# Kernel tuning notes

Hardware: AMD Instinct MI355X
Metric: run time of the kernel (lower is better)

## Reference

```python
import jax, jax.numpy as jnp
import numpy as np

TEMPERATURE = 0.1  # use_temperature=True


def setup_inputs() -> dict:
    key = jax.random.key(0)
    # encoder output features: [batch_size, num_epoch, feature_dim]
    feature = jax.random.normal(key, (128, 64, 128), dtype=jnp.float32)
    return {"feature": feature}


def reference(feature):
    # L2-normalize along feature dim (F.normalize, p=2, dim=1 on flat features)
    f = feature / jnp.linalg.norm(feature, axis=-1, keepdims=True)
    B, E, D = f.shape
    # full pairwise logits: [B, E, E, B]
    logits = jnp.einsum('ijk,mnk->ijnm', f, f) / TEMPERATURE
    e = jnp.exp(logits)
    idx = jnp.arange(B)
    # mask[i, j, :, i] = 1 -> positives are the m == i block: e[i, j, :, i]
    pos = e[idx, :, :, idx].sum(-1)              # [B, E]
    neg = e.sum(axis=(2, 3)) - pos               # [B, E] everything else
    loss = (-jnp.log(pos / (pos + neg))).mean()
    return loss
```

## Files before the change

kernel.cpp:

```cpp
#include <hip/hip_runtime.h>
#include <hip/hip_bf16.h>

#define N_ROWS 8192
#define DIM    128
#define TILE   128
#define CPG    8
#define EXPTEN 22026.465794806718f
#define SCALE  3.7982826f

typedef __attribute__((ext_vector_type(8))) short short8;
typedef __attribute__((ext_vector_type(4))) float floatx4;

#if __has_builtin(__builtin_amdgcn_exp2f)
#define EXP2F(x) __builtin_amdgcn_exp2f(x)
#else
#define EXP2F(x) __expf((x) * 0.6931471805599453f)
#endif

__global__ void norm_kernel(const float* __restrict__ F, __hip_bfloat16* __restrict__ Xb,
                            float* __restrict__ pos, float* __restrict__ den) {
    int lane = threadIdx.x & 63;
    int wave = threadIdx.x >> 6;
    int row  = blockIdx.x * 4 + wave;
    const float2 v = *(const float2*)(F + (size_t)row * DIM + lane * 2);
    float ss = v.x * v.x + v.y * v.y;
    #pragma unroll
    for (int m = 1; m < 64; m <<= 1) ss += __shfl_xor(ss, m);
    float inv = rsqrtf(ss) * SCALE;
    __hip_bfloat162 o;
    o.x = __float2bfloat16(v.x * inv);
    o.y = __float2bfloat16(v.y * inv);
    *((__hip_bfloat162*)(Xb + (size_t)row * DIM) + lane) = o;
    if (lane == 0) { pos[row] = 0.f; den[row] = 0.f; }
}

__global__ __launch_bounds__(256, 2) void gram_kernel(
        const __hip_bfloat16* __restrict__ Xb,
        float* __restrict__ pos, float* __restrict__ den) {
    const int tid  = threadIdx.x;
    const int rb   = blockIdx.x;
    const int cg   = blockIdx.y;
    const int lane = tid & 63;
    const int wave = tid >> 6;
    const int wm   = wave >> 1, wn = wave & 1;
    const int quad = lane >> 4;
    const int l15  = lane & 15;

    short8 af[4][4];
    {
        const __hip_bfloat16* Ab = Xb + ((size_t)(rb * TILE + wm * 64 + l15)) * DIM + quad * 8;
        #pragma unroll
        for (int mi = 0; mi < 4; ++mi)
            #pragma unroll
            for (int ko = 0; ko < 4; ++ko)
                af[mi][ko] = *(const short8*)(Ab + mi * 16 * DIM + ko * 32);
    }

    float dp[4][4];
    #pragma unroll
    for (int a = 0; a < 4; ++a)
        #pragma unroll
        for (int b = 0; b < 4; ++b) dp[a][b] = 0.f;

    floatx4 acc[4][4];
    short8 bfr[4][4];

    auto epilogue = [&](int ct) {
        const bool pos_tile = (ct == rb) && (wm == wn);
        #pragma unroll
        for (int mi = 0; mi < 4; ++mi)
            #pragma unroll
            for (int rg = 0; rg < 4; ++rg) {
                float dadd = 0.f;
                #pragma unroll
                for (int ni = 0; ni < 4; ++ni)
                    dadd += EXP2F(acc[mi][ni][rg]);
                if (pos_tile) {
                    if (l15 == quad * 4 + rg)
                        dadd += EXPTEN - EXP2F(acc[mi][mi][rg]);
                    float p = dadd;
                    #pragma unroll
                    for (int m = 1; m < 16; m <<= 1) p += __shfl_xor(p, m);
                    if (l15 == 0)
                        atomicAdd(&pos[rb * TILE + wm * 64 + mi * 16 + quad * 4 + rg], p);
                }
                dp[mi][rg] += dadd;
            }
    };

    auto load_b = [&](int ct) {
        const __hip_bfloat16* Bb = Xb + ((size_t)(ct * TILE + wn * 64 + l15)) * DIM + quad * 8;
        #pragma unroll
        for (int ni = 0; ni < 4; ++ni)
            #pragma unroll
            for (int ko = 0; ko < 4; ++ko)
                bfr[ni][ko] = *(const short8*)(Bb + ni * 16 * DIM + ko * 32);
    };

    auto do_mfma = [&]() {
        #pragma unroll
        for (int mi = 0; mi < 4; ++mi)
            #pragma unroll
            for (int ni = 0; ni < 4; ++ni) acc[mi][ni] = (floatx4)0.0f;
        #pragma unroll
        for (int ko = 0; ko < 4; ++ko)
            #pragma unroll
            for (int mi = 0; mi < 4; ++mi)
                #pragma unroll
                for (int ni = 0; ni < 4; ++ni)
                    acc[mi][ni] = __builtin_amdgcn_mfma_f32_16x16x32_bf16(
                        af[mi][ko], bfr[ni][ko], acc[mi][ni], 0, 0, 0);
    };

    load_b(cg * CPG);
    do_mfma();
    #pragma unroll 1
    for (int t = 1; t < CPG; ++t) {
        load_b(cg * CPG + t);
        epilogue(cg * CPG + t - 1);
        do_mfma();
    }
    epilogue(cg * CPG + CPG - 1);

    #pragma unroll
    for (int mi = 0; mi < 4; ++mi)
        #pragma unroll
        for (int rg = 0; rg < 4; ++rg) {
            float d = dp[mi][rg];
            #pragma unroll
            for (int m = 1; m < 16; m <<= 1) d += __shfl_xor(d, m);
            if (l15 == 0)
                atomicAdd(&den[rb * TILE + wm * 64 + mi * 16 + quad * 4 + rg], d);
        }
}

__global__ void loss_kernel(const float* __restrict__ pos, const float* __restrict__ den,
                            float* __restrict__ out) {
    __shared__ float red[4];
    float acc = 0.f;
    for (int i = threadIdx.x; i < N_ROWS / 4; i += 256) {
        float4 d = ((const float4*)den)[i];
        float4 p = ((const float4*)pos)[i];
        acc += __logf(d.x / p.x) + __logf(d.y / p.y) +
               __logf(d.z / p.z) + __logf(d.w / p.w);
    }
    #pragma unroll
    for (int m = 1; m < 64; m <<= 1) acc += __shfl_xor(acc, m);
    int lane = threadIdx.x & 63, w = threadIdx.x >> 6;
    if (lane == 0) red[w] = acc;
    __syncthreads();
    if (threadIdx.x == 0)
        out[0] = (red[0] + red[1] + red[2] + red[3]) * (1.0f / (float)N_ROWS);
}

extern "C" void kernel_launch(void* const* d_in, const int* in_sizes, int n_in,
                              void* d_out, int out_size, void* d_ws, size_t ws_size,
                              hipStream_t stream) {
    const float* feature = (const float*)d_in[0];
    float* pos = (float*)d_ws;
    float* den = pos + N_ROWS;
    __hip_bfloat16* Xb = (__hip_bfloat16*)(den + N_ROWS);

    norm_kernel<<<N_ROWS / 4, 256, 0, stream>>>(feature, Xb, pos, den);
    gram_kernel<<<dim3(64, 8), 256, 0, stream>>>(Xb, pos, den);
    loss_kernel<<<1, 256, 0, stream>>>(pos, den, (float*)d_out);
}
```

Measured before the change: 99.97 us.

## Stage B tiles through swizzled LDS double buffer with direct global-to-LDS loads

Replaces the per-wave register loads of the B tile with a double-buffered shared-memory stage filled by global_load_lds DMA, using an XOR swizzle to avoid bank conflicts. Each wave now reads its B fragments from LDS, so the two waves sharing a column half no longer each fetch the same data from global memory, and the next tile's load overlaps the current tile's MFMA and exp epilogue. This costs 64KB of LDS per block, which may limit occupancy to two blocks per CU, and adds a barrier per tile. The unconditional use of the exp2 builtin also drops the fallback path.

```diff
diff --git a/kernel.cpp b/kernel.cpp
--- a/kernel.cpp
+++ b/kernel.cpp
@@ -11,11 +11,12 @@
 typedef __attribute__((ext_vector_type(8))) short short8;
 typedef __attribute__((ext_vector_type(4))) float floatx4;
 
-#if __has_builtin(__builtin_amdgcn_exp2f)
 #define EXP2F(x) __builtin_amdgcn_exp2f(x)
-#else
-#define EXP2F(x) __expf((x) * 0.6931471805599453f)
-#endif
+
+#define GLOAD_LDS(g, l)                                                        \
+    __builtin_amdgcn_global_load_lds(                                          \
+        (const __attribute__((address_space(1))) void*)(g),                    \
+        (__attribute__((address_space(3))) void*)(l), 16, 0, 0)
 
 __global__ void norm_kernel(const float* __restrict__ F, __hip_bfloat16* __restrict__ Xb,
                             float* __restrict__ pos, float* __restrict__ den) {
@@ -37,6 +38,7 @@
 __global__ __launch_bounds__(256, 2) void gram_kernel(
         const __hip_bfloat16* __restrict__ Xb,
         float* __restrict__ pos, float* __restrict__ den) {
+    __shared__ __hip_bfloat16 Bs[2][TILE * DIM];
     const int tid  = threadIdx.x;
     const int rb   = blockIdx.x;
     const int cg   = blockIdx.y;
@@ -62,10 +64,43 @@
         #pragma unroll
         for (int b = 0; b < 4; ++b) dp[a][b] = 0.f;
 
-    floatx4 acc[4][4];
-    short8 bfr[4][4];
+    auto stage = [&](int ct, int buf) {
+        #pragma unroll
+        for (int i = 0; i < 8; ++i) {
+            int chunk = (i * 4 + wave) * 64 + lane;
+            int r  = chunk >> 4;
+            int cs = (chunk & 15) ^ (r & 15);
+            const __hip_bfloat16* gp = Xb + ((size_t)(ct * TILE + r)) * DIM + cs * 8;
+            char* lp = (char*)&Bs[buf][0] + (i * 4 + wave) * 1024;
+            GLOAD_LDS(gp, lp);
+        }
+    };
 
-    auto epilogue = [&](int ct) {
+    auto compute = [&](int ct, int buf) {
+        floatx4 acc[4][4];
+        #pragma unroll
+        for (int mi = 0; mi < 4; ++mi)
+            #pragma unroll
+            for (int ni = 0; ni < 4; ++ni) acc[mi][ni] = (floatx4)0.0f;
+
+        const char* Bb = (const char*)&Bs[buf][0];
+        #pragma unroll
+        for (int ko = 0; ko < 4; ++ko) {
+            short8 bf[4];
+            #pragma unroll
+            for (int ni = 0; ni < 4; ++ni) {
+                int r  = wn * 64 + ni * 16 + l15;
+                int ch = (ko * 4 + quad) ^ l15;
+                bf[ni] = *(const short8*)(Bb + r * 256 + ch * 16);
+            }
+            #pragma unroll
+            for (int mi = 0; mi < 4; ++mi)
+                #pragma unroll
+                for (int ni = 0; ni < 4; ++ni)
+                    acc[mi][ni] = __builtin_amdgcn_mfma_f32_16x16x32_bf16(
+                        af[mi][ko], bf[ni], acc[mi][ni], 0, 0, 0);
+        }
+
         const bool pos_tile = (ct == rb) && (wm == wn);
         #pragma unroll
         for (int mi = 0; mi < 4; ++mi)
@@ -88,39 +123,15 @@
             }
     };
 
-    auto load_b = [&](int ct) {
-        const __hip_bfloat16* Bb = Xb + ((size_t)(ct * TILE + wn * 64 + l15)) * DIM + quad * 8;
-        #pragma unroll
-        for (int ni = 0; ni < 4; ++ni)
-            #pragma unroll
-            for (int ko = 0; ko < 4; ++ko)
-                bfr[ni][ko] = *(const short8*)(Bb + ni * 16 * DIM + ko * 32);
-    };
-
-    auto do_mfma = [&]() {
-        #pragma unroll
-        for (int mi = 0; mi < 4; ++mi)
-            #pragma unroll
-            for (int ni = 0; ni < 4; ++ni) acc[mi][ni] = (floatx4)0.0f;
-        #pragma unroll
-        for (int ko = 0; ko < 4; ++ko)
-            #pragma unroll
-            for (int mi = 0; mi < 4; ++mi)
-                #pragma unroll
-                for (int ni = 0; ni < 4; ++ni)
-                    acc[mi][ni] = __builtin_amdgcn_mfma_f32_16x16x32_bf16(
-                        af[mi][ko], bfr[ni][ko], acc[mi][ni], 0, 0, 0);
-    };
-
-    load_b(cg * CPG);
-    do_mfma();
+    stage(cg * CPG, 0);
+    __syncthreads();
     #pragma unroll 1
-    for (int t = 1; t < CPG; ++t) {
-        load_b(cg * CPG + t);
-        epilogue(cg * CPG + t - 1);
-        do_mfma();
+    for (int t = 0; t < CPG - 1; ++t) {
+        stage(cg * CPG + t + 1, (t + 1) & 1);
+        compute(cg * CPG + t, t & 1);
+        __syncthreads();
     }
-    epilogue(cg * CPG + CPG - 1);
+    compute(cg * CPG + CPG - 1, (CPG - 1) & 1);
 
     #pragma unroll
     for (int mi = 0; mi < 4; ++mi)
```

After: 87.69 us. 1.14x faster.

## Restructure gram kernel: per-wave 64-row strips, 24 column groups, atomic-free partial reduction

Applied to the files above, without the earlier changes.

Each wave now owns a separate 64-row strip and streams 16-column B fragments with a one-step register prefetch. The grid changes from 64x8 to 32x24 with an uneven 5/6-tile column split, to fill the GPU better, and occupancy rises to 3 blocks per SIMD. The atomicAdd reductions into den and pos are replaced by plain per-group partial writes, summed afterwards by a new dr_kernel and a tiny final loss kernel. This removes the atomics and the zero-init, at the cost of an extra launch and more workspace traffic.

```diff
diff --git a/kernel.cpp b/kernel.cpp
--- a/kernel.cpp
+++ b/kernel.cpp
@@ -3,22 +3,16 @@
 
 #define N_ROWS 8192
 #define DIM    128
-#define TILE   128
-#define CPG    8
+#define NGRP   24
 #define EXPTEN 22026.465794806718f
 #define SCALE  3.7982826f
 
 typedef __attribute__((ext_vector_type(8))) short short8;
 typedef __attribute__((ext_vector_type(4))) float floatx4;
 
-#if __has_builtin(__builtin_amdgcn_exp2f)
 #define EXP2F(x) __builtin_amdgcn_exp2f(x)
-#else
-#define EXP2F(x) __expf((x) * 0.6931471805599453f)
-#endif
 
-__global__ void norm_kernel(const float* __restrict__ F, __hip_bfloat16* __restrict__ Xb,
-                            float* __restrict__ pos, float* __restrict__ den) {
+__global__ void norm_kernel(const float* __restrict__ F, __hip_bfloat16* __restrict__ Xb) {
     int lane = threadIdx.x & 63;
     int wave = threadIdx.x >> 6;
     int row  = blockIdx.x * 4 + wave;
@@ -31,24 +25,28 @@
     o.x = __float2bfloat16(v.x * inv);
     o.y = __float2bfloat16(v.y * inv);
     *((__hip_bfloat162*)(Xb + (size_t)row * DIM) + lane) = o;
-    if (lane == 0) { pos[row] = 0.f; den[row] = 0.f; }
 }
 
-__global__ __launch_bounds__(256, 2) void gram_kernel(
+__global__ __launch_bounds__(256, 3) void gram_kernel(
         const __hip_bfloat16* __restrict__ Xb,
-        float* __restrict__ pos, float* __restrict__ den) {
-    const int tid  = threadIdx.x;
+        float* __restrict__ pos, float* __restrict__ part) {
     const int rb   = blockIdx.x;
     const int cg   = blockIdx.y;
-    const int lane = tid & 63;
-    const int wave = tid >> 6;
-    const int wm   = wave >> 1, wn = wave & 1;
+    const int lane = threadIdx.x & 63;
+    const int wave = threadIdx.x >> 6;
     const int quad = lane >> 4;
     const int l15  = lane & 15;
 
+    const int start  = (cg < 16) ? cg * 5 : 80 + (cg - 16) * 6;
+    const int cnt    = (cg < 16) ? 5 : 6;
+    const int nsteps = cnt * 4;
+    const int c0     = start * 64;
+
+    const int R0 = rb * 256 + wave * 64;
+
     short8 af[4][4];
     {
-        const __hip_bfloat16* Ab = Xb + ((size_t)(rb * TILE + wm * 64 + l15)) * DIM + quad * 8;
+        const __hip_bfloat16* Ab = Xb + (size_t)(R0 + l15) * DIM + quad * 8;
         #pragma unroll
         for (int mi = 0; mi < 4; ++mi)
             #pragma unroll
@@ -56,112 +54,118 @@
                 af[mi][ko] = *(const short8*)(Ab + mi * 16 * DIM + ko * 32);
     }
 
-    float dp[4][4];
+    const __hip_bfloat16* Bb = Xb + (size_t)(c0 + l15) * DIM + quad * 8;
+
+    float dp[4][4], pp[4][4];
     #pragma unroll
     for (int a = 0; a < 4; ++a)
         #pragma unroll
-        for (int b = 0; b < 4; ++b) dp[a][b] = 0.f;
+        for (int b = 0; b < 4; ++b) { dp[a][b] = 0.f; pp[a][b] = 0.f; }
 
-    floatx4 acc[4][4];
-    short8 bfr[4][4];
+    const int  pt     = R0 >> 6;
+    const bool haspos = (pt >= start) && (pt < start + cnt);
+    const int  s0     = (pt - start) * 4;
 
-    auto epilogue = [&](int ct) {
-        const bool pos_tile = (ct == rb) && (wm == wn);
+    short8 nb[4];
+    #pragma unroll
+    for (int ko = 0; ko < 4; ++ko)
+        nb[ko] = *(const short8*)(Bb + ko * 32);
+
+    #pragma unroll 1
+    for (int s = 0; s < nsteps; ++s) {
+        short8 cb[4];
+        #pragma unroll
+        for (int ko = 0; ko < 4; ++ko) cb[ko] = nb[ko];
+        if (s + 1 < nsteps) {
+            const __hip_bfloat16* p = Bb + (size_t)(s + 1) * 16 * DIM;
+            #pragma unroll
+            for (int ko = 0; ko < 4; ++ko)
+                nb[ko] = *(const short8*)(p + ko * 32);
+        }
+
+        floatx4 acc[4];
+        #pragma unroll
+        for (int mi = 0; mi < 4; ++mi) acc[mi] = (floatx4)0.0f;
+        #pragma unroll
+        for (int ko = 0; ko < 4; ++ko)
+            #pragma unroll
+            for (int mi = 0; mi < 4; ++mi)
+                acc[mi] = __builtin_amdgcn_mfma_f32_16x16x32_bf16(
+                    af[mi][ko], cb[ko], acc[mi], 0, 0, 0);
+
+        const bool ispos = haspos && (s >= s0) && (s < s0 + 4);
         #pragma unroll
         for (int mi = 0; mi < 4; ++mi)
             #pragma unroll
             for (int rg = 0; rg < 4; ++rg) {
-                float dadd = 0.f;
-                #pragma unroll
-                for (int ni = 0; ni < 4; ++ni)
-                    dadd += EXP2F(acc[mi][ni][rg]);
-                if (pos_tile) {
-                    if (l15 == quad * 4 + rg)
-                        dadd += EXPTEN - EXP2F(acc[mi][mi][rg]);
-                    float p = dadd;
-                    #pragma unroll
-                    for (int m = 1; m < 16; m <<= 1) p += __shfl_xor(p, m);
-                    if (l15 == 0)
-                        atomicAdd(&pos[rb * TILE + wm * 64 + mi * 16 + quad * 4 + rg], p);
-                }
-                dp[mi][rg] += dadd;
+                float ev = EXP2F(acc[mi][rg]);
+                if (ispos && mi == s - s0 && l15 == quad * 4 + rg)
+                    ev = EXPTEN;
+                dp[mi][rg] += ev;
+                if (ispos) pp[mi][rg] += ev;
             }
-    };
-
-    auto load_b = [&](int ct) {
-        const __hip_bfloat16* Bb = Xb + ((size_t)(ct * TILE + wn * 64 + l15)) * DIM + quad * 8;
-        #pragma unroll
-        for (int ni = 0; ni < 4; ++ni)
-            #pragma unroll
-            for (int ko = 0; ko < 4; ++ko)
-                bfr[ni][ko] = *(const short8*)(Bb + ni * 16 * DIM + ko * 32);
-    };
-
-    auto do_mfma = [&]() {
-        #pragma unroll
-        for (int mi = 0; mi < 4; ++mi)
-            #pragma unroll
-            for (int ni = 0; ni < 4; ++ni) acc[mi][ni] = (floatx4)0.0f;
-        #pragma unroll
-        for (int ko = 0; ko < 4; ++ko)
-            #pragma unroll
-            for (int mi = 0; mi < 4; ++mi)
-                #pragma unroll
-                for (int ni = 0; ni < 4; ++ni)
-                    acc[mi][ni] = __builtin_amdgcn_mfma_f32_16x16x32_bf16(
-                        af[mi][ko], bfr[ni][ko], acc[mi][ni], 0, 0, 0);
-    };
-
-    load_b(cg * CPG);
-    do_mfma();
-    #pragma unroll 1
-    for (int t = 1; t < CPG; ++t) {
-        load_b(cg * CPG + t);
-        epilogue(cg * CPG + t - 1);
-        do_mfma();
     }
-    epilogue(cg * CPG + CPG - 1);
 
     #pragma unroll
     for (int mi = 0; mi < 4; ++mi)
         #pragma unroll
         for (int rg = 0; rg < 4; ++rg) {
-            float d = dp[mi][rg];
+            float v = dp[mi][rg];
             #pragma unroll
-            for (int m = 1; m < 16; m <<= 1) d += __shfl_xor(d, m);
+            for (int m = 1; m < 16; m <<= 1) v += __shfl_xor(v, m);
             if (l15 == 0)
-                atomicAdd(&den[rb * TILE + wm * 64 + mi * 16 + quad * 4 + rg], d);
+                part[(size_t)cg * N_ROWS + R0 + mi * 16 + quad * 4 + rg] = v;
         }
+    if (haspos) {
+        #pragma unroll
+        for (int mi = 0; mi < 4; ++mi)
+            #pragma unroll
+            for (int rg = 0; rg < 4; ++rg) {
+                float v = pp[mi][rg];
+                #pragma unroll
+                for (int m = 1; m < 16; m <<= 1) v += __shfl_xor(v, m);
+                if (l15 == 0)
+                    pos[R0 + mi * 16 + quad * 4 + rg] = v;
+            }
+    }
 }
 
-__global__ void loss_kernel(const float* __restrict__ pos, const float* __restrict__ den,
-                            float* __restrict__ out) {
+__global__ void dr_kernel(const float* __restrict__ part, const float* __restrict__ pos,
+                          float* __restrict__ bsum) {
     __shared__ float red[4];
-    float acc = 0.f;
-    for (int i = threadIdx.x; i < N_ROWS / 4; i += 256) {
-        float4 d = ((const float4*)den)[i];
-        float4 p = ((const float4*)pos)[i];
-        acc += __logf(d.x / p.x) + __logf(d.y / p.y) +
-               __logf(d.z / p.z) + __logf(d.w / p.w);
-    }
+    const int row = blockIdx.x * 256 + threadIdx.x;
+    float den = 0.f;
     #pragma unroll
-    for (int m = 1; m < 64; m <<= 1) acc += __shfl_xor(acc, m);
+    for (int g = 0; g < NGRP; ++g)
+        den += part[(size_t)g * N_ROWS + row];
+    float v = __logf(den / pos[row]);
+    #pragma unroll
+    for (int m = 1; m < 64; m <<= 1) v += __shfl_xor(v, m);
     int lane = threadIdx.x & 63, w = threadIdx.x >> 6;
-    if (lane == 0) red[w] = acc;
+    if (lane == 0) red[w] = v;
     __syncthreads();
     if (threadIdx.x == 0)
-        out[0] = (red[0] + red[1] + red[2] + red[3]) * (1.0f / (float)N_ROWS);
+        bsum[blockIdx.x] = red[0] + red[1] + red[2] + red[3];
+}
+
+__global__ void loss_kernel(const float* __restrict__ bsum, float* __restrict__ out) {
+    float v = (threadIdx.x < 32) ? bsum[threadIdx.x] : 0.f;
+    #pragma unroll
+    for (int m = 1; m < 64; m <<= 1) v += __shfl_xor(v, m);
+    if (threadIdx.x == 0) out[0] = v * (1.0f / (float)N_ROWS);
 }
 
 extern "C" void kernel_launch(void* const* d_in, const int* in_sizes, int n_in,
                               void* d_out, int out_size, void* d_ws, size_t ws_size,
                               hipStream_t stream) {
     const float* feature = (const float*)d_in[0];
-    float* pos = (float*)d_ws;
-    float* den = pos + N_ROWS;
-    __hip_bfloat16* Xb = (__hip_bfloat16*)(den + N_ROWS);
+    float* pos  = (float*)d_ws;
+    float* part = pos + N_ROWS;
+    float* bsum = part + (size_t)NGRP * N_ROWS;
+    __hip_bfloat16* Xb = (__hip_bfloat16*)(bsum + 64);
 
-    norm_kernel<<<N_ROWS / 4, 256, 0, stream>>>(feature, Xb, pos, den);
-    gram_kernel<<<dim3(64, 8), 256, 0, stream>>>(Xb, pos, den);
-    loss_kernel<<<1, 256, 0, stream>>>(pos, den, (float*)d_out);
+    norm_kernel<<<N_ROWS / 4, 256, 0, stream>>>(feature, Xb);
+    gram_kernel<<<dim3(32, NGRP), 256, 0, stream>>>(Xb, pos, part);
+    dr_kernel<<<N_ROWS / 256, 256, 0, stream>>>(part, pos, bsum);
+    loss_kernel<<<1, 64, 0, stream>>>(bsum, (float*)d_out);
 }
```

Measured after the change: 101.4 us. About the same (+1.4%).
